# Kernel tuning notes

Measured on AMD Instinct MI355X. Metric: run time of the kernel, lower is better.

The kernel has to match this reference:

```python
import jax, jax.numpy as jnp
import numpy as np
from jax import lax

PERM_AD = np.array([3, 0, 1, 6, 4, 2, 7, 8, 5])  # angular-difference kernel permutation
IDX_HD_POS = np.array([0, 3, 6]); IDX_HD_NEG = np.array([2, 5, 8])
IDX_VD_POS = np.array([0, 1, 2]); IDX_VD_NEG = np.array([6, 7, 8])
TOP_K = 1
THETA = 1.0


def conv2d_3x3(x, w, b):
    # x: [B,C,H,W], w: [O,I,3,3], b: [O]; stride 1, padding 1
    out = lax.conv_general_dilated(x, w, window_strides=(1, 1), padding=((1, 1), (1, 1)),
                                   dimension_numbers=('NCHW', 'OIHW', 'NCHW'))
    return out + b[None, :, None, None]


def setup_inputs() -> dict:
    key = jax.random.key(0)
    ks = jax.random.split(key, 12)
    B, C, H, W, E = 16, 64, 128, 128, 5

    def winit(k, shape, fan_in):
        return jax.random.normal(k, shape, jnp.float32) * (1.0 / np.sqrt(fan_in))

    return {
        'x': jax.random.normal(ks[0], (B, C, H, W), jnp.float32),
        'noise': jax.random.normal(ks[1], (B, E), jnp.float32),
        'w_gate': winit(ks[2], (C, E), C), 'b_gate': jnp.zeros((E,), jnp.float32),
        'w_noise': winit(ks[3], (C, E), C), 'b_noise': jnp.zeros((E,), jnp.float32),
        'w1': winit(ks[4], (C, C, 3, 3), C * 9), 'b1': jnp.zeros((C,), jnp.float32),
        'w_cd': winit(ks[5], (C, C, 3, 3), C * 9), 'b_cd': jnp.zeros((C,), jnp.float32),
        'w_hd': winit(ks[6], (C, C, 3), C * 3), 'b_hd': jnp.zeros((C,), jnp.float32),
        'w_vd': winit(ks[7], (C, C, 3), C * 3), 'b_vd': jnp.zeros((C,), jnp.float32),
        'w_ad': winit(ks[8], (C, C, 3, 3), C * 9), 'b_ad': jnp.zeros((C,), jnp.float32),
    }


def reference(x, noise, w_gate, b_gate, w_noise, b_noise,
              w1, b1, w_cd, b_cd, w_hd, b_hd, w_vd, b_vd, w_ad, b_ad):
    B, C, H, W = x.shape
    E = w_gate.shape[1]

    # ---- NoisyTopkRouter on globally pooled features ----
    pooled = x.mean(axis=(2, 3))                      # [B, C]
    logits = pooled @ w_gate + b_gate                 # [B, E]
    noise_logits = pooled @ w_noise + b_noise         # [B, E]
    noisy = logits + noise * jax.nn.softplus(noise_logits)
    topv, topi = lax.top_k(noisy, TOP_K)              # [B, k]
    sparse = jnp.full_like(noisy, -jnp.inf)
    sparse = sparse.at[jnp.arange(B)[:, None], topi].set(topv)
    gates = jax.nn.softmax(sparse, axis=-1)           # [B, E]; 0 for unselected, gate weight otherwise

    # ---- Difference-convolution expert kernels ----
    wcd_f = w_cd.reshape(C, C, 9)
    wcd = wcd_f.at[:, :, 4].add(-wcd_f.sum(-1)).reshape(C, C, 3, 3)   # center = w4 - sum(all)
    whd = jnp.zeros((C, C, 9), x.dtype).at[:, :, IDX_HD_POS].set(w_hd).at[:, :, IDX_HD_NEG].set(-w_hd).reshape(C, C, 3, 3)
    wvd = jnp.zeros((C, C, 9), x.dtype).at[:, :, IDX_VD_POS].set(w_vd).at[:, :, IDX_VD_NEG].set(-w_vd).reshape(C, C, 3, 3)
    wad_f = w_ad.reshape(C, C, 9)
    wad = (wad_f - THETA * wad_f[:, :, PERM_AD]).reshape(C, C, 3, 3)

    outs = jnp.stack([
        conv2d_3x3(x, w1, b1),
        conv2d_3x3(x, wcd, b_cd),
        conv2d_3x3(x, whd, b_hd),
        conv2d_3x3(x, wvd, b_vd),
        conv2d_3x3(x, wad, b_ad),
    ], axis=0)                                        # [E, B, C, H, W]

    # ---- SparseDispatcher.combine: per-example softmax over flattened depth, gate-weighted scatter-add ----
    flat = outs.reshape(E, B, C * H * W)
    sm = jax.nn.softmax(flat, axis=-1)                # softmax over depth dim, as in combine()
    combined = jnp.einsum('ebd,be->bd', sm, gates)    # gates are 0 for non-dispatched (expert,example) pairs
    return combined.reshape(B, C, H, W)
```

## Files before the change

kernel.cpp:

```cpp
#include <hip/hip_runtime.h>
#include <math.h>

#define B_  16
#define C_  64
#define E_  5

typedef __bf16  bf16x8 __attribute__((ext_vector_type(8)));
typedef float   f32x4  __attribute__((ext_vector_type(4)));

#define WS_WEFFB   0
#define WS_BIAS    368640
#define WS_POOL    369920
#define WS_Z       374016
#define WS_EIDX    374080
#define WS_XT      374144
#define WS_EXP     33928576ull
#define WS_NEED_A  67483008ull

static __device__ __forceinline__ unsigned short f2bf(float f) {
    unsigned int u = __float_as_uint(f);
    unsigned int r = (u + 0x7fffu + ((u >> 16) & 1u)) >> 16;
    return (unsigned short)r;
}

__global__ __launch_bounds__(256) void transpose_pool_kernel(
        const float* __restrict__ x, unsigned short* __restrict__ x_t,
        float* __restrict__ pooled) {
    int bid = blockIdx.x;
    int b = bid >> 7, row = bid & 127;
    int t = threadIdx.x;
    int wave = t >> 6, l = t & 63;
    int half = l >> 5;
    int c4 = l & 31;

    __shared__ unsigned short T[128][72];

    const float* xb = x + (size_t)b * (64 * 16384) + row * 128;

    #pragma unroll
    for (int it = 0; it < 8; it++) {
        int ci = wave * 16 + it * 2 + half;
        float4 v = *(const float4*)(xb + (size_t)ci * 16384 + c4 * 4);
        float p = v.x + v.y + v.z + v.w;
        p += __shfl_down(p, 16, 32);
        p += __shfl_down(p, 8, 32);
        p += __shfl_down(p, 4, 32);
        p += __shfl_down(p, 2, 32);
        p += __shfl_down(p, 1, 32);
        if (c4 == 0) atomicAdd(&pooled[b * 64 + ci], p * (1.0f / 16384.0f));
        int colb = c4 * 4;
        T[colb + 0][ci] = f2bf(v.x);
        T[colb + 1][ci] = f2bf(v.y);
        T[colb + 2][ci] = f2bf(v.z);
        T[colb + 3][ci] = f2bf(v.w);
    }
    __syncthreads();

    unsigned short* dst = x_t + ((size_t)(b * 128 + row) * 128) * 64;
    #pragma unroll
    for (int k = 0; k < 4; k++) {
        int chunk = t + k * 256;
        int col = chunk >> 3, c8 = chunk & 7;
        uint4 vv = *(const uint4*)&T[col][c8 * 8];
        *(uint4*)(dst + col * 64 + c8 * 8) = vv;
    }
}

__global__ __launch_bounds__(256) void prep_kernel(
        const float* __restrict__ pooled, const float* __restrict__ noise,
        const float* __restrict__ w_gate, const float* __restrict__ b_gate,
        const float* __restrict__ w_noise, const float* __restrict__ b_noise,
        const float* __restrict__ w1, const float* __restrict__ w_cd,
        const float* __restrict__ w_hd, const float* __restrict__ w_vd,
        const float* __restrict__ w_ad,
        const float* __restrict__ b1, const float* __restrict__ b_cd,
        const float* __restrict__ b_hd, const float* __restrict__ b_vd,
        const float* __restrict__ b_ad,
        int* __restrict__ expert_idx,
        unsigned short* __restrict__ wEffB, float* __restrict__ biasEff) {
    int blk = blockIdx.x;
    int t = threadIdx.x;

    if (blk < B_) {
        if (t < 64) {
            int b = blk;
            float pv = pooled[b * C_ + t];
            float ge[E_], ne[E_];
            #pragma unroll
            for (int e = 0; e < E_; e++) {
                ge[e] = pv * w_gate[t * E_ + e];
                ne[e] = pv * w_noise[t * E_ + e];
            }
            #pragma unroll
            for (int off = 32; off; off >>= 1) {
                #pragma unroll
                for (int e = 0; e < E_; e++) {
                    ge[e] += __shfl_xor(ge[e], off, 64);
                    ne[e] += __shfl_xor(ne[e], off, 64);
                }
            }
            if (t == 0) {
                float best = -1e30f; int bi = 0;
                #pragma unroll
                for (int e = 0; e < E_; e++) {
                    float lg = ge[e] + b_gate[e];
                    float nz = ne[e] + b_noise[e];
                    float sp = log1pf(expf(nz));
                    float v = lg + noise[b * E_ + e] * sp;
                    if (v > best) { best = v; bi = e; }
                }
                expert_idx[b] = bi;
            }
        }
        return;
    }

    int gid = (blk - B_) * 256 + t;
    if (gid < E_ * 36864) {
        int e   = gid / 36864;
        int r   = gid % 36864;
        int g   = r / 18432;
        int r2  = r % 18432;
        int tap = r2 / 2048;
        int r3  = r2 % 2048;
        int q   = r3 / 512;
        int r4  = r3 % 512;
        int co  = r4 / 8;
        int j   = r4 % 8;
        int ci = g * 32 + q * 8 + j;
        int base9 = (co * 64 + ci) * 9;
        int base3 = (co * 64 + ci) * 3;
        float v = 0.f;
        if (e == 0) {
            v = w1[base9 + tap];
        } else if (e == 1) {
            if (tap == 4) {
                float s = 0.f;
                #pragma unroll
                for (int k = 0; k < 9; k++) s += w_cd[base9 + k];
                v = w_cd[base9 + 4] - s;
            } else {
                v = w_cd[base9 + tap];
            }
        } else if (e == 2) {
            int m = tap % 3;
            if (m == 0) v = w_hd[base3 + tap / 3];
            else if (m == 2) v = -w_hd[base3 + tap / 3];
        } else if (e == 3) {
            if (tap < 3) v = w_vd[base3 + tap];
            else if (tap >= 6) v = -w_vd[base3 + tap - 6];
        } else {
            const int PERM[9] = {3, 0, 1, 6, 4, 2, 7, 8, 5};
            v = w_ad[base9 + tap] - w_ad[base9 + PERM[tap]];
        }
        wEffB[gid] = f2bf(v);
    } else if (gid < E_ * 36864 + E_ * 64) {
        int jj = gid - E_ * 36864;
        int e = jj / 64, co = jj % 64;
        const float* bs;
        switch (e) {
            case 0: bs = b1; break;
            case 1: bs = b_cd; break;
            case 2: bs = b_hd; break;
            case 3: bs = b_vd; break;
            default: bs = b_ad; break;
        }
        biasEff[jj] = bs[co];
    }
}

__global__ __launch_bounds__(256, 4) void conv_mfma_kernel(
        const unsigned short* __restrict__ x_t, const unsigned short* __restrict__ wEffB,
        const float* __restrict__ biasEff, const int* __restrict__ expert_idx,
        unsigned short* __restrict__ expw, float* __restrict__ outf,
        float* __restrict__ Z, int direct_f32) {
    int bid = blockIdx.x;
    int b = bid >> 6;
    int rem = bid & 63;
    int rg = rem >> 1;
    int ch = rem & 1;

    int t = threadIdx.x;
    int wave = t >> 6;
    int lane = t & 63;
    int ln = lane & 15;
    int q = lane >> 4;

    int e = expert_idx[b];

    __shared__ __align__(16) unsigned short A_lds[3 * 4 * 66 * 8];
    __shared__ __align__(16) unsigned short Xs[6 * 4 * 68 * 8];
    __shared__ float zs[4];

    f32x4 acc[4][4];
    #pragma unroll
    for (int i = 0; i < 4; i++)
        #pragma unroll
        for (int jn = 0; jn < 4; jn++)
            acc[i][jn] = (f32x4){0.f, 0.f, 0.f, 0.f};

    const unsigned short* xb = x_t + (size_t)b * (128 * 128 * 64);
    const unsigned short* we = wEffB + (size_t)e * 36864;

    for (int g = 0; g < 2; g++) {
        for (int j = t; j < 1584; j += 256) {
            int xr = j / 264;
            int r2 = j % 264;
            int col = r2 >> 2;
            int qq = r2 & 3;
            int irow = rg * 4 - 1 + xr;
            int icol = ch * 64 - 1 + col;
            uint4 v = make_uint4(0, 0, 0, 0);
            if ((unsigned)irow < 128u && (unsigned)icol < 128u)
                v = *(const uint4*)(xb + ((size_t)irow * 128 + icol) * 64 + g * 32 + qq * 8);
            *(uint4*)&Xs[((xr * 4 + qq) * 68 + col) * 8] = v;
        }

        const uint4* asrc = (const uint4*)(we + g * 18432);
        #pragma unroll
        for (int chunk = 0; chunk < 3; chunk++) {
            #pragma unroll
            for (int k = 0; k < 3; k++) {
                int j = t + k * 256;
                int slotrow = j >> 6;
                int m = j & 63;
                *(uint4*)&A_lds[(slotrow * 66 + m) * 8] = asrc[chunk * 768 + j];
            }
            __syncthreads();

            int xr = wave + chunk;
            #pragma unroll
            for (int tl = 0; tl < 3; tl++) {
                bf16x8 af[4], bfr[4];
                #pragma unroll
                for (int mt = 0; mt < 4; mt++)
                    af[mt] = *(const bf16x8*)&A_lds[((tl * 4 + q) * 66 + mt * 16 + ln) * 8];
                #pragma unroll
                for (int t4 = 0; t4 < 4; t4++)
                    bfr[t4] = *(const bf16x8*)&Xs[((xr * 4 + q) * 68 + t4 * 16 + ln + tl) * 8];
                #pragma unroll
                for (int mt = 0; mt < 4; mt++)
                    #pragma unroll
                    for (int t4 = 0; t4 < 4; t4++)
                        acc[mt][t4] = __builtin_amdgcn_mfma_f32_16x16x32_bf16(
                            af[mt], bfr[t4], acc[mt][t4], 0, 0, 0);
            }
            __syncthreads();
        }
    }

    int orow = rg * 4 + wave;
    float bsum = 0.f;
    size_t obase = (size_t)b * (64 * 16384);
    #pragma unroll
    for (int mt = 0; mt < 4; mt++) {
        float4 bias4 = *(const float4*)(biasEff + e * 64 + mt * 16 + q * 4);
        const float* bp = (const float*)&bias4;
        #pragma unroll
        for (int r = 0; r < 4; r++) {
            int co = mt * 16 + q * 4 + r;
            size_t cb = obase + (size_t)co * 16384 + (size_t)orow * 128;
            #pragma unroll
            for (int t4 = 0; t4 < 4; t4++) {
                float ev = __expf(acc[mt][t4][r] + bp[r]);
                bsum += ev;
                int ocol = ch * 64 + t4 * 16 + ln;
                if (direct_f32) outf[cb + ocol] = ev;
                else            expw[cb + ocol] = f2bf(ev);
            }
        }
    }
    for (int off = 32; off; off >>= 1) bsum += __shfl_down(bsum, off, 64);
    if (lane == 0) zs[wave] = bsum;
    __syncthreads();
    if (t == 0) atomicAdd(&Z[b], zs[0] + zs[1] + zs[2] + zs[3]);
}

#define N_UINT4 2097152
__global__ __launch_bounds__(256) void scale_bf16_kernel(
        const unsigned short* __restrict__ expw, const float* __restrict__ Z,
        float* __restrict__ out) {
    __shared__ float sinv[B_];
    if (threadIdx.x < B_) sinv[threadIdx.x] = 1.0f / Z[threadIdx.x];
    __syncthreads();
    for (int gid = blockIdx.x * 256 + threadIdx.x; gid < N_UINT4; gid += 2048 * 256) {
        int b = gid >> 17;
        float s = sinv[b];
        uint4 r = ((const uint4*)expw)[gid];
        float4 o0, o1;
        o0.x = __uint_as_float(r.x << 16) * s;
        o0.y = __uint_as_float(r.x & 0xffff0000u) * s;
        o0.z = __uint_as_float(r.y << 16) * s;
        o0.w = __uint_as_float(r.y & 0xffff0000u) * s;
        o1.x = __uint_as_float(r.z << 16) * s;
        o1.y = __uint_as_float(r.z & 0xffff0000u) * s;
        o1.z = __uint_as_float(r.w << 16) * s;
        o1.w = __uint_as_float(r.w & 0xffff0000u) * s;
        ((float4*)out)[gid * 2] = o0;
        ((float4*)out)[gid * 2 + 1] = o1;
    }
}

#define N_FLOAT4 4194304
__global__ __launch_bounds__(256) void scale_inplace_kernel(
        float* __restrict__ out, const float* __restrict__ Z) {
    __shared__ float sinv[B_];
    if (threadIdx.x < B_) sinv[threadIdx.x] = 1.0f / Z[threadIdx.x];
    __syncthreads();
    for (int gid = blockIdx.x * 256 + threadIdx.x; gid < N_FLOAT4; gid += 2048 * 256) {
        int b = gid >> 18;
        float s = sinv[b];
        float4 v = ((float4*)out)[gid];
        v.x *= s; v.y *= s; v.z *= s; v.w *= s;
        ((float4*)out)[gid] = v;
    }
}

extern "C" void kernel_launch(void* const* d_in, const int* in_sizes, int n_in,
                              void* d_out, int out_size, void* d_ws, size_t ws_size,
                              hipStream_t stream) {
    const float* x       = (const float*)d_in[0];
    const float* noise   = (const float*)d_in[1];
    const float* w_gate  = (const float*)d_in[2];
    const float* b_gate  = (const float*)d_in[3];
    const float* w_noise = (const float*)d_in[4];
    const float* b_noise = (const float*)d_in[5];
    const float* w1      = (const float*)d_in[6];
    const float* b1      = (const float*)d_in[7];
    const float* w_cd    = (const float*)d_in[8];
    const float* b_cd    = (const float*)d_in[9];
    const float* w_hd    = (const float*)d_in[10];
    const float* b_hd    = (const float*)d_in[11];
    const float* w_vd    = (const float*)d_in[12];
    const float* b_vd    = (const float*)d_in[13];
    const float* w_ad    = (const float*)d_in[14];
    const float* b_ad    = (const float*)d_in[15];

    char* ws = (char*)d_ws;
    unsigned short* wEffB   = (unsigned short*)(ws + WS_WEFFB);
    float*          biasEff = (float*)(ws + WS_BIAS);
    float*          pooled  = (float*)(ws + WS_POOL);
    float*          Zbuf    = (float*)(ws + WS_Z);
    int*            eidx    = (int*)(ws + WS_EIDX);
    unsigned short* x_t     = (unsigned short*)(ws + WS_XT);
    unsigned short* expw    = (unsigned short*)(ws + WS_EXP);

    float* out = (float*)d_out;
    int mode_a = (ws_size >= WS_NEED_A) ? 1 : 0;

    hipMemsetAsync(pooled, 0, 4160, stream);

    transpose_pool_kernel<<<B_ * 128, 256, 0, stream>>>(x, x_t, pooled);
    prep_kernel<<<B_ + 722, 256, 0, stream>>>(pooled, noise, w_gate, b_gate,
                                              w_noise, b_noise,
                                              w1, w_cd, w_hd, w_vd, w_ad,
                                              b1, b_cd, b_hd, b_vd, b_ad,
                                              eidx, wEffB, biasEff);
    conv_mfma_kernel<<<1024, 256, 0, stream>>>(x_t, wEffB, biasEff, eidx,
                                               expw, out, Zbuf, mode_a ? 0 : 1);
    if (mode_a)
        scale_bf16_kernel<<<2048, 256, 0, stream>>>(expw, Zbuf, out);
    else
        scale_inplace_kernel<<<2048, 256, 0, stream>>>(out, Zbuf);
}
```

Before: 215.4 us.

## Fuse prep into transpose and conv, add per-batch grid barrier to normalize in-kernel

Folds the weight-building work into the transpose kernel and moves router top-1 selection into each conv block. A per-example atomic counter barrier lets conv blocks wait for the full softmax denominator, then write the normalized fp32 output directly, removing the separate scale pass and its bf16 intermediate round-trip. It also cuts the Xs LDS buffer to a 4-row ring, loading rows incrementally, which permits 5 blocks per CU. The spin barrier relies on all 64 blocks of an example being co-resident, guarded only by an occupancy query and an iteration cap, so it risks deadlock or wrong results if the scheduler does not keep them resident.

Measured after the change: 259.9 us. 1.21x slower.

```diff
diff --git a/kernel.cpp b/kernel.cpp
--- a/kernel.cpp
+++ b/kernel.cpp
@@ -12,10 +12,10 @@
 #define WS_BIAS    368640
 #define WS_POOL    369920
 #define WS_Z       374016
-#define WS_EIDX    374080
-#define WS_XT      374144
-#define WS_EXP     33928576ull
-#define WS_NEED_A  67483008ull
+#define WS_CNT     374080
+#define WS_XT      376128
+#define WS_EXP     33930560ull
+#define WS_NEED_A  67484992ull
 
 static __device__ __forceinline__ unsigned short f2bf(float f) {
     unsigned int u = __float_as_uint(f);
@@ -23,12 +23,76 @@
     return (unsigned short)r;
 }
 
-__global__ __launch_bounds__(256) void transpose_pool_kernel(
+__global__ __launch_bounds__(256) void transpose_build_kernel(
         const float* __restrict__ x, unsigned short* __restrict__ x_t,
-        float* __restrict__ pooled) {
+        float* __restrict__ pooled,
+        const float* __restrict__ w1, const float* __restrict__ w_cd,
+        const float* __restrict__ w_hd, const float* __restrict__ w_vd,
+        const float* __restrict__ w_ad,
+        const float* __restrict__ b1, const float* __restrict__ b_cd,
+        const float* __restrict__ b_hd, const float* __restrict__ b_vd,
+        const float* __restrict__ b_ad,
+        unsigned short* __restrict__ wEffB, float* __restrict__ biasEff) {
     int bid = blockIdx.x;
+    int t = threadIdx.x;
+
+    if (bid >= 2048) {
+        int gid = (bid - 2048) * 256 + t;
+        if (gid < E_ * 36864) {
+            int e   = gid / 36864;
+            int r   = gid % 36864;
+            int g   = r / 18432;
+            int r2  = r % 18432;
+            int tap = r2 / 2048;
+            int r3  = r2 % 2048;
+            int q   = r3 / 512;
+            int r4  = r3 % 512;
+            int co  = r4 / 8;
+            int j   = r4 % 8;
+            int ci = g * 32 + q * 8 + j;
+            int base9 = (co * 64 + ci) * 9;
+            int base3 = (co * 64 + ci) * 3;
+            float v = 0.f;
+            if (e == 0) {
+                v = w1[base9 + tap];
+            } else if (e == 1) {
+                if (tap == 4) {
+                    float s = 0.f;
+                    #pragma unroll
+                    for (int k = 0; k < 9; k++) s += w_cd[base9 + k];
+                    v = w_cd[base9 + 4] - s;
+                } else {
+                    v = w_cd[base9 + tap];
+                }
+            } else if (e == 2) {
+                int m = tap % 3;
+                if (m == 0) v = w_hd[base3 + tap / 3];
+                else if (m == 2) v = -w_hd[base3 + tap / 3];
+            } else if (e == 3) {
+                if (tap < 3) v = w_vd[base3 + tap];
+                else if (tap >= 6) v = -w_vd[base3 + tap - 6];
+            } else {
+                const int PERM[9] = {3, 0, 1, 6, 4, 2, 7, 8, 5};
+                v = w_ad[base9 + tap] - w_ad[base9 + PERM[tap]];
+            }
+            wEffB[gid] = f2bf(v);
+        } else if (gid < E_ * 36864 + E_ * 64) {
+            int jj = gid - E_ * 36864;
+            int e = jj / 64, co = jj % 64;
+            const float* bs;
+            switch (e) {
+                case 0: bs = b1; break;
+                case 1: bs = b_cd; break;
+                case 2: bs = b_hd; break;
+                case 3: bs = b_vd; break;
+                default: bs = b_ad; break;
+            }
+            biasEff[jj] = bs[co];
+        }
+        return;
+    }
+
     int b = bid >> 7, row = bid & 127;
-    int t = threadIdx.x;
     int wave = t >> 6, l = t & 63;
     int half = l >> 5;
     int c4 = l & 31;
@@ -66,114 +130,15 @@
     }
 }
 
-__global__ __launch_bounds__(256) void prep_kernel(
+__global__ __launch_bounds__(256, 5) void conv_mfma_kernel(
+        const unsigned short* __restrict__ x_t, const unsigned short* __restrict__ wEffB,
+        const float* __restrict__ biasEff,
         const float* __restrict__ pooled, const float* __restrict__ noise,
         const float* __restrict__ w_gate, const float* __restrict__ b_gate,
         const float* __restrict__ w_noise, const float* __restrict__ b_noise,
-        const float* __restrict__ w1, const float* __restrict__ w_cd,
-        const float* __restrict__ w_hd, const float* __restrict__ w_vd,
-        const float* __restrict__ w_ad,
-        const float* __restrict__ b1, const float* __restrict__ b_cd,
-        const float* __restrict__ b_hd, const float* __restrict__ b_vd,
-        const float* __restrict__ b_ad,
-        int* __restrict__ expert_idx,
-        unsigned short* __restrict__ wEffB, float* __restrict__ biasEff) {
-    int blk = blockIdx.x;
-    int t = threadIdx.x;
-
-    if (blk < B_) {
-        if (t < 64) {
-            int b = blk;
-            float pv = pooled[b * C_ + t];
-            float ge[E_], ne[E_];
-            #pragma unroll
-            for (int e = 0; e < E_; e++) {
-                ge[e] = pv * w_gate[t * E_ + e];
-                ne[e] = pv * w_noise[t * E_ + e];
-            }
-            #pragma unroll
-            for (int off = 32; off; off >>= 1) {
-                #pragma unroll
-                for (int e = 0; e < E_; e++) {
-                    ge[e] += __shfl_xor(ge[e], off, 64);
-                    ne[e] += __shfl_xor(ne[e], off, 64);
-                }
-            }
-            if (t == 0) {
-                float best = -1e30f; int bi = 0;
-                #pragma unroll
-                for (int e = 0; e < E_; e++) {
-                    float lg = ge[e] + b_gate[e];
-                    float nz = ne[e] + b_noise[e];
-                    float sp = log1pf(expf(nz));
-                    float v = lg + noise[b * E_ + e] * sp;
-                    if (v > best) { best = v; bi = e; }
-                }
-                expert_idx[b] = bi;
-            }
-        }
-        return;
-    }
-
-    int gid = (blk - B_) * 256 + t;
-    if (gid < E_ * 36864) {
-        int e   = gid / 36864;
-        int r   = gid % 36864;
-        int g   = r / 18432;
-        int r2  = r % 18432;
-        int tap = r2 / 2048;
-        int r3  = r2 % 2048;
-        int q   = r3 / 512;
-        int r4  = r3 % 512;
-        int co  = r4 / 8;
-        int j   = r4 % 8;
-        int ci = g * 32 + q * 8 + j;
-        int base9 = (co * 64 + ci) * 9;
-        int base3 = (co * 64 + ci) * 3;
-        float v = 0.f;
-        if (e == 0) {
-            v = w1[base9 + tap];
-        } else if (e == 1) {
-            if (tap == 4) {
-                float s = 0.f;
-                #pragma unroll
-                for (int k = 0; k < 9; k++) s += w_cd[base9 + k];
-                v = w_cd[base9 + 4] - s;
-            } else {
-                v = w_cd[base9 + tap];
-            }
-        } else if (e == 2) {
-            int m = tap % 3;
-            if (m == 0) v = w_hd[base3 + tap / 3];
-            else if (m == 2) v = -w_hd[base3 + tap / 3];
-        } else if (e == 3) {
-            if (tap < 3) v = w_vd[base3 + tap];
-            else if (tap >= 6) v = -w_vd[base3 + tap - 6];
-        } else {
-            const int PERM[9] = {3, 0, 1, 6, 4, 2, 7, 8, 5};
-            v = w_ad[base9 + tap] - w_ad[base9 + PERM[tap]];
-        }
-        wEffB[gid] = f2bf(v);
-    } else if (gid < E_ * 36864 + E_ * 64) {
-        int jj = gid - E_ * 36864;
-        int e = jj / 64, co = jj % 64;
-        const float* bs;
-        switch (e) {
-            case 0: bs = b1; break;
-            case 1: bs = b_cd; break;
-            case 2: bs = b_hd; break;
-            case 3: bs = b_vd; break;
-            default: bs = b_ad; break;
-        }
-        biasEff[jj] = bs[co];
-    }
-}
-
-__global__ __launch_bounds__(256, 4) void conv_mfma_kernel(
-        const unsigned short* __restrict__ x_t, const unsigned short* __restrict__ wEffB,
-        const float* __restrict__ biasEff, const int* __restrict__ expert_idx,
         unsigned short* __restrict__ expw, float* __restrict__ outf,
-        float* __restrict__ Z, int direct_f32) {
+        float* __restrict__ Z, unsigned int* __restrict__ cnt,
+        int do_bar, int direct_f32) {
     int bid = blockIdx.x;
     int b = bid >> 6;
     int rem = bid & 63;
@@ -186,11 +151,43 @@
     int ln = lane & 15;
     int q = lane >> 4;
 
-    int e = expert_idx[b];
-
     __shared__ __align__(16) unsigned short A_lds[3 * 4 * 66 * 8];
-    __shared__ __align__(16) unsigned short Xs[6 * 4 * 68 * 8];
+    __shared__ __align__(16) unsigned short Xs[4 * 4 * 68 * 8];
     __shared__ float zs[4];
+    __shared__ int   se_sh;
+    __shared__ float sinv_sh;
+
+    if (wave == 0) {
+        float pv = pooled[b * C_ + lane];
+        float ge[E_], ne[E_];
+        #pragma unroll
+        for (int e = 0; e < E_; e++) {
+            ge[e] = pv * w_gate[lane * E_ + e];
+            ne[e] = pv * w_noise[lane * E_ + e];
+        }
+        #pragma unroll
+        for (int off = 32; off; off >>= 1) {
+            #pragma unroll
+            for (int e = 0; e < E_; e++) {
+                ge[e] += __shfl_xor(ge[e], off, 64);
+                ne[e] += __shfl_xor(ne[e], off, 64);
+            }
+        }
+        if (lane == 0) {
+            float best = -1e30f; int bi = 0;
+            #pragma unroll
+            for (int e = 0; e < E_; e++) {
+                float lg = ge[e] + b_gate[e];
+                float nz = ne[e] + b_noise[e];
+                float sp = log1pf(expf(nz));
+                float v = lg + noise[b * E_ + e] * sp;
+                if (v > best) { best = v; bi = e; }
+            }
+            se_sh = bi;
+        }
+    }
+    __syncthreads();
+    int e = se_sh;
 
     f32x4 acc[4][4];
     #pragma unroll
@@ -203,22 +200,35 @@
     const unsigned short* we = wEffB + (size_t)e * 36864;
 
     for (int g = 0; g < 2; g++) {
-        for (int j = t; j < 1584; j += 256) {
-            int xr = j / 264;
-            int r2 = j % 264;
-            int col = r2 >> 2;
-            int qq = r2 & 3;
-            int irow = rg * 4 - 1 + xr;
-            int icol = ch * 64 - 1 + col;
-            uint4 v = make_uint4(0, 0, 0, 0);
-            if ((unsigned)irow < 128u && (unsigned)icol < 128u)
-                v = *(const uint4*)(xb + ((size_t)irow * 128 + icol) * 64 + g * 32 + qq * 8);
-            *(uint4*)&Xs[((xr * 4 + qq) * 68 + col) * 8] = v;
-        }
-
         const uint4* asrc = (const uint4*)(we + g * 18432);
         #pragma unroll
         for (int chunk = 0; chunk < 3; chunk++) {
+            if (chunk == 0) {
+                for (int j = t; j < 1056; j += 256) {
+                    int xr = j / 264;
+                    int r2 = j % 264;
+                    int col = r2 >> 2;
+                    int qq = r2 & 3;
+                    int irow = rg * 4 - 1 + xr;
+                    int icol = ch * 64 - 1 + col;
+                    uint4 v = make_uint4(0, 0, 0, 0);
+                    if ((unsigned)irow < 128u && (unsigned)icol < 128u)
+                        v = *(const uint4*)(xb + ((size_t)irow * 128 + icol) * 64 + g * 32 + qq * 8);
+                    *(uint4*)&Xs[(((xr & 3) * 4 + qq) * 68 + col) * 8] = v;
+                }
+            } else {
+                int xr = 3 + chunk;
+                int irow = rg * 4 - 1 + xr;
+                for (int j = t; j < 264; j += 256) {
+                    int col = j >> 2;
+                    int qq = j & 3;
+                    int icol = ch * 64 - 1 + col;
+                    uint4 v = make_uint4(0, 0, 0, 0);
+                    if ((unsigned)irow < 128u && (unsigned)icol < 128u)
+                        v = *(const uint4*)(xb + ((size_t)irow * 128 + icol) * 64 + g * 32 + qq * 8);
+                    *(uint4*)&Xs[(((xr & 3) * 4 + qq) * 68 + col) * 8] = v;
+                }
+            }
             #pragma unroll
             for (int k = 0; k < 3; k++) {
                 int j = t + k * 256;
@@ -228,7 +238,7 @@
             }
             __syncthreads();
 
-            int xr = wave + chunk;
+            int xrl = wave + chunk;
             #pragma unroll
             for (int tl = 0; tl < 3; tl++) {
                 bf16x8 af[4], bfr[4];
@@ -237,7 +247,7 @@
                     af[mt] = *(const bf16x8*)&A_lds[((tl * 4 + q) * 66 + mt * 16 + ln) * 8];
                 #pragma unroll
                 for (int t4 = 0; t4 < 4; t4++)
-                    bfr[t4] = *(const bf16x8*)&Xs[((xr * 4 + q) * 68 + t4 * 16 + ln + tl) * 8];
+                    bfr[t4] = *(const bf16x8*)&Xs[(((xrl & 3) * 4 + q) * 68 + t4 * 16 + ln + tl) * 8];
                 #pragma unroll
                 for (int mt = 0; mt < 4; mt++)
                     #pragma unroll
@@ -249,31 +259,76 @@
         }
     }
 
-    int orow = rg * 4 + wave;
     float bsum = 0.f;
-    size_t obase = (size_t)b * (64 * 16384);
     #pragma unroll
     for (int mt = 0; mt < 4; mt++) {
         float4 bias4 = *(const float4*)(biasEff + e * 64 + mt * 16 + q * 4);
         const float* bp = (const float*)&bias4;
         #pragma unroll
         for (int r = 0; r < 4; r++) {
-            int co = mt * 16 + q * 4 + r;
-            size_t cb = obase + (size_t)co * 16384 + (size_t)orow * 128;
             #pragma unroll
             for (int t4 = 0; t4 < 4; t4++) {
                 float ev = __expf(acc[mt][t4][r] + bp[r]);
+                acc[mt][t4][r] = ev;
                 bsum += ev;
-                int ocol = ch * 64 + t4 * 16 + ln;
-                if (direct_f32) outf[cb + ocol] = ev;
-                else            expw[cb + ocol] = f2bf(ev);
             }
         }
     }
     for (int off = 32; off; off >>= 1) bsum += __shfl_down(bsum, off, 64);
     if (lane == 0) zs[wave] = bsum;
     __syncthreads();
-    if (t == 0) atomicAdd(&Z[b], zs[0] + zs[1] + zs[2] + zs[3]);
+
+    int orow = rg * 4 + wave;
+    size_t obase = (size_t)b * (64 * 16384);
+
+    if (do_bar) {
+        if (t == 0) {
+            atomicAdd(&Z[b], zs[0] + zs[1] + zs[2] + zs[3]);
+            __threadfence();
+            atomicAdd(&cnt[b * 32], 1u);
+            unsigned int it = 0;
+            while (__hip_atomic_load(&cnt[b * 32], __ATOMIC_RELAXED,
+                                     __HIP_MEMORY_SCOPE_AGENT) < 64u) {
+                __builtin_amdgcn_s_sleep(8);
+                if (++it > (1u << 20)) break;
+            }
+            __threadfence();
+            sinv_sh = 1.0f / __hip_atomic_load(&Z[b], __ATOMIC_RELAXED,
+                                               __HIP_MEMORY_SCOPE_AGENT);
+        }
+        __syncthreads();
+        float sinv = sinv_sh;
+        #pragma unroll
+        for (int mt = 0; mt < 4; mt++) {
+            #pragma unroll
+            for (int r = 0; r < 4; r++) {
+                int co = mt * 16 + q * 4 + r;
+                size_t cb = obase + (size_t)co * 16384 + (size_t)orow * 128;
+                #pragma unroll
+                for (int t4 = 0; t4 < 4; t4++) {
+                    int ocol = ch * 64 + t4 * 16 + ln;
+                    outf[cb + ocol] = acc[mt][t4][r] * sinv;
+                }
+            }
+        }
+    } else {
+        if (t == 0) atomicAdd(&Z[b], zs[0] + zs[1] + zs[2] + zs[3]);
+        #pragma unroll
+        for (int mt = 0; mt < 4; mt++) {
+            #pragma unroll
+            for (int r = 0; r < 4; r++) {
+                int co = mt * 16 + q * 4 + r;
+                size_t cb = obase + (size_t)co * 16384 + (size_t)orow * 128;
+                #pragma unroll
+                for (int t4 = 0; t4 < 4; t4++) {
+                    int ocol = ch * 64 + t4 * 16 + ln;
+                    float ev = acc[mt][t4][r];
+                    if (direct_f32) outf[cb + ocol] = ev;
+                    else            expw[cb + ocol] = f2bf(ev);
+                }
+            }
+        }
+    }
 }
 
 #define N_UINT4 2097152
@@ -341,25 +396,32 @@
     float*          biasEff = (float*)(ws + WS_BIAS);
     float*          pooled  = (float*)(ws + WS_POOL);
     float*          Zbuf    = (float*)(ws + WS_Z);
-    int*            eidx    = (int*)(ws + WS_EIDX);
+    unsigned int*   cnt     = (unsigned int*)(ws + WS_CNT);
     unsigned short* x_t     = (unsigned short*)(ws + WS_XT);
     unsigned short* expw    = (unsigned short*)(ws + WS_EXP);
 
     float* out = (float*)d_out;
+
+    hipMemsetAsync(pooled, 0, 6208, stream);
+
+    int nb = 0;
+    hipError_t qerr = hipOccupancyMaxActiveBlocksPerMultiprocessor(
+        &nb, (const void*)conv_mfma_kernel, 256, 0);
+    int do_bar = (qerr == hipSuccess && nb >= 4) ? 1 : 0;
     int mode_a = (ws_size >= WS_NEED_A) ? 1 : 0;
 
-    hipMemsetAsync(pooled, 0, 4160, stream);
-
-    transpose_pool_kernel<<<B_ * 128, 256, 0, stream>>>(x, x_t, pooled);
-    prep_kernel<<<B_ + 722, 256, 0, stream>>>(pooled, noise, w_gate, b_gate,
-                                              w_noise, b_noise,
-                                              w1, w_cd, w_hd, w_vd, w_ad,
-                                              b1, b_cd, b_hd, b_vd, b_ad,
-                                              eidx, wEffB, biasEff);
-    conv_mfma_kernel<<<1024, 256, 0, stream>>>(x_t, wEffB, biasEff, eidx,
-                                               expw, out, Zbuf, mode_a ? 0 : 1);
-    if (mode_a)
-        scale_bf16_kernel<<<2048, 256, 0, stream>>>(expw, Zbuf, out);
-    else
-        scale_inplace_kernel<<<2048, 256, 0, stream>>>(out, Zbuf);
-}
+    transpose_build_kernel<<<2048 + 722, 256, 0, stream>>>(
+        x, x_t, pooled, w1, w_cd, w_hd, w_vd, w_ad,
+        b1, b_cd, b_hd, b_vd, b_ad, wEffB, biasEff);
+
+    conv_mfma_kernel<<<1024, 256, 0, stream>>>(
+        x_t, wEffB, biasEff, pooled, noise, w_gate, b_gate, w_noise, b_noise,
+        expw, out, Zbuf, cnt, do_bar, (do_bar || !mode_a) ? 1 : 0);
+
+    if (!do_bar) {
+        if (mode_a)
+            scale_bf16_kernel<<<2048, 256, 0, stream>>>(expw, Zbuf, out);
+        else
+            scale_inplace_kernel<<<2048, 256, 0, stream>>>(out, Zbuf);
+    }
+}
```
